# Kernel tuning notes

Hardware: AMD Instinct MI355X
Metric: run time of the kernel (lower is better)

## Reference

```python
import jax, jax.numpy as jnp
import numpy as np

ALIBI_SLOPES = jnp.array([0.6299605249, 0.396850263, 0.25, 0.1574901312,
                          0.0992125657, 0.0625, 0.0393725328, 0.0248031414,
                          0.015625, 0.0098431332, 0.0062007854, 0.00390625],
                         dtype=jnp.float32)
H, D = 12, 64
SCALE = D ** (-0.5)


def setup_inputs() -> dict:
    key = jax.random.key(0)
    ks = jax.random.split(key, 9)
    B, S, E = 4, 2048, 768
    s = 0.02
    return {
        "x": jax.random.normal(ks[0], (B, S, E), dtype=jnp.float32),
        "Wq": jax.random.normal(ks[1], (E, E), dtype=jnp.float32) * s,
        "bq": jnp.zeros((E,), dtype=jnp.float32),
        "Wk": jax.random.normal(ks[2], (E, E), dtype=jnp.float32) * s,
        "bk": jnp.zeros((E,), dtype=jnp.float32),
        "Wv": jax.random.normal(ks[3], (E, E), dtype=jnp.float32) * s,
        "bv": jnp.zeros((E,), dtype=jnp.float32),
        "Wo": jax.random.normal(ks[4], (E, E), dtype=jnp.float32) * s,
        "bo": jnp.zeros((E,), dtype=jnp.float32),
    }


def reference(x, Wq, bq, Wk, bk, Wv, bv, Wo, bo):
    B, S, E = x.shape
    # projections (weights stored input-major: y = x @ W + b)
    q = (x @ Wq + bq).reshape(B, S, H, D).transpose(0, 2, 1, 3)  # [B,H,S,D]
    k = (x @ Wk + bk).reshape(B, S, H, D).transpose(0, 2, 1, 3)
    v = (x @ Wv + bv).reshape(B, S, H, D).transpose(0, 2, 1, 3)

    scores = jnp.einsum('bhqd,bhkd->bhqk', q, k) * SCALE  # [B,H,S,S]

    pos = jnp.arange(S, dtype=jnp.float32)
    a = ALIBI_SLOPES[:, None] * pos[None, :]          # [H,S]
    alibi = a[:, :, None] - a[:, None, :]             # [H,S,S]
    scores = scores + alibi[None]

    causal = jnp.triu(jnp.ones((S, S), dtype=bool), k=1)  # True above diag
    scores = jnp.where(causal[None, None], -jnp.inf, scores)

    attn = jax.nn.softmax(scores, axis=-1)
    o = jnp.einsum('bhqk,bhkd->bhqd', attn, v)  # [B,H,S,D]

    # Faithful to original: view of contiguous (B,H,S,D) buffer as (B,S,E)
    # (head-major flatten, reproducing the original module's reshape).
    o = o.reshape(B, S, E)
    return o @ Wo + bo
```

## Files before the change

### kernel.cpp

```cpp
#include <hip/hip_runtime.h>
#include <hip/hip_bf16.h>
#include <cstdint>
#include <cstddef>

#define B_ 4
#define S_ 2048
#define E_ 768
#define H_ 12
#define D_ 64

typedef __bf16 bf16x8 __attribute__((ext_vector_type(8)));
typedef float f32x4 __attribute__((ext_vector_type(4)));

__constant__ float c_slopes[12] = {
    0.6299605249f, 0.396850263f, 0.25f, 0.1574901312f,
    0.0992125657f, 0.0625f, 0.0393725328f, 0.0248031414f,
    0.015625f, 0.0098431332f, 0.0062007854f, 0.00390625f};

__device__ __forceinline__ unsigned short f2bf_u(float f) {
    unsigned u = __builtin_bit_cast(unsigned, f);
    u += 0x7fffu + ((u >> 16) & 1u);
    return (unsigned short)(u >> 16);
}
__device__ __forceinline__ __bf16 f2bf(float f) {
    unsigned short s = f2bf_u(f);
    return __builtin_bit_cast(__bf16, s);
}

__device__ __forceinline__ void gload_lds16(const void* g, void* l) {
    __builtin_amdgcn_global_load_lds(
        (const __attribute__((address_space(1))) unsigned int*)g,
        (__attribute__((address_space(3))) unsigned int*)l, 16, 0, 0);
}

__global__ __launch_bounds__(256) void prep(
    const float* __restrict__ x, __bf16* __restrict__ xb,
    const float* __restrict__ W0, const float* __restrict__ W1,
    const float* __restrict__ W2, const float* __restrict__ W3,
    __bf16* __restrict__ Wt) {
    __shared__ alignas(16) __bf16 ts[64 * 72];
    const int L = blockIdx.x;
    const int t = threadIdx.x;
    if (L < 6144) {
        int i = (L * 256 + t) * 4;
        float4 v = *(const float4*)(x + i);
        ushort4 o;
        o.x = f2bf_u(v.x); o.y = f2bf_u(v.y); o.z = f2bf_u(v.z); o.w = f2bf_u(v.w);
        *(ushort4*)((unsigned short*)xb + i) = o;
        return;
    }
    const int id = L - 6144;
    const int z = id / 144, rem = id % 144;
    const int k0 = (rem / 12) * 64, n0 = (rem % 12) * 64;
    const float* W = z == 0 ? W0 : z == 1 ? W1 : z == 2 ? W2 : W3;
    __bf16* out = Wt + (size_t)z * E_ * E_;
#pragma unroll
    for (int i = 0; i < 4; i++) {
        int idx = i * 256 + t;
        int row = idx >> 4, c4 = idx & 15;
        float4 v = *(const float4*)(W + (size_t)(k0 + row) * E_ + n0 + c4 * 4);
        ts[(c4 * 4 + 0) * 72 + row] = f2bf(v.x);
        ts[(c4 * 4 + 1) * 72 + row] = f2bf(v.y);
        ts[(c4 * 4 + 2) * 72 + row] = f2bf(v.z);
        ts[(c4 * 4 + 3) * 72 + row] = f2bf(v.w);
    }
    __syncthreads();
#pragma unroll
    for (int i = 0; i < 2; i++) {
        int idx = i * 256 + t;
        int r = idx >> 3, c8 = idx & 7;
        *(uint4*)((unsigned short*)out + (size_t)(n0 + r) * E_ + k0 + c8 * 8) =
            *(const uint4*)((const unsigned short*)ts + r * 72 + c8 * 8);
    }
}

__global__ __launch_bounds__(256, 3) void qkv_gemm(
    const __bf16* __restrict__ A, const __bf16* __restrict__ WtAll,
    const float* __restrict__ b0, const float* __restrict__ b1,
    const float* __restrict__ b2, __bf16* __restrict__ Qb,
    __bf16* __restrict__ Kb, __bf16* __restrict__ Vtb) {
    constexpr int Kd = E_;
    __shared__ alignas(16) __bf16 Asm[2][128 * 32];
    __shared__ alignas(16) __bf16 Bsm[2][3][64 * 32];

    const int t = threadIdx.x;
    const int w = t >> 6, lane = t & 63;
    const int qm = lane & 15, quad = lane >> 4;
    const int m0 = blockIdx.y * 128, n0 = blockIdx.x * 64;
    const int wm = w * 32;

    float bvv[3][4];
    const float* bs[3] = {b0, b1, b2};
#pragma unroll
    for (int z = 0; z < 3; z++)
#pragma unroll
        for (int j = 0; j < 4; j++) bvv[z][j] = bs[z][n0 + j * 16 + qm];

    const int crow = lane >> 2;
    const int ccol = lane & 3;

    f32x4 acc[3][2][4] = {};

    for (int k0 = 0; k0 < Kd; k0 += 64) {
#pragma unroll
        for (int p = 0; p < 2; p++) {
            const int kp = k0 + p * 32;
#pragma unroll
            for (int cc = 0; cc < 2; cc++) {
                int chunk = w * 2 + cc;
                gload_lds16((const unsigned short*)A +
                                (size_t)(m0 + chunk * 16 + crow) * Kd + kp + ccol * 8,
                            Asm[p] + chunk * 512);
            }
#pragma unroll
            for (int e = 0; e < 3; e++) {
                int g = w * 3 + e;
                int z = g >> 2, cz = g & 3;
                gload_lds16((const unsigned short*)WtAll + (size_t)z * Kd * E_ +
                                (size_t)(n0 + cz * 16 + crow) * Kd + kp + ccol * 8,
                            Bsm[p][z] + cz * 512);
            }
        }
        __syncthreads();

#pragma unroll
        for (int p = 0; p < 2; p++) {
            bf16x8 af[2];
#pragma unroll
            for (int i = 0; i < 2; i++)
                af[i] = *(const bf16x8*)(Asm[p] + (wm + i * 16 + qm) * 32 + quad * 8);
#pragma unroll
            for (int z = 0; z < 3; z++) {
                bf16x8 bg[4];
#pragma unroll
                for (int j = 0; j < 4; j++)
                    bg[j] = *(const bf16x8*)(Bsm[p][z] + (j * 16 + qm) * 32 + quad * 8);
#pragma unroll
                for (int i = 0; i < 2; i++)
#pragma unroll
                    for (int j = 0; j < 4; j++)
                        acc[z][i][j] = __builtin_amdgcn_mfma_f32_16x16x32_bf16(
                            af[i], bg[j], acc[z][i][j], 0, 0, 0);
            }
        }
        __syncthreads();
    }

#pragma unroll
    for (int z = 0; z < 3; z++) {
        __bf16* out = z == 0 ? Qb : z == 1 ? Kb : Vtb;
#pragma unroll
        for (int i = 0; i < 2; i++) {
#pragma unroll
            for (int j = 0; j < 4; j++) {
                int col = n0 + j * 16 + qm;
                int rowb = m0 + wm + i * 16 + quad * 4;
                int h = col >> 6, d = col & (D_ - 1);
                if (z == 2) {
                    int b = rowb >> 11, s = rowb & (S_ - 1);
                    unsigned short pk4[4];
#pragma unroll
                    for (int r = 0; r < 4; r++)
                        pk4[r] = f2bf_u(acc[z][i][j][r] + bvv[z][j]);
                    uint2 pv;
                    pv.x = (unsigned)pk4[0] | ((unsigned)pk4[1] << 16);
                    pv.y = (unsigned)pk4[2] | ((unsigned)pk4[3] << 16);
                    *(uint2*)((unsigned short*)out +
                              ((size_t)(b * H_ + h) * D_ + d) * S_ + s) = pv;
                } else {
#pragma unroll
                    for (int r = 0; r < 4; r++) {
                        int row = rowb + r;
                        int b = row >> 11, s = row & (S_ - 1);
                        out[(((size_t)(b * H_ + h)) * S_ + s) * D_ + d] =
                            f2bf(acc[z][i][j][r] + bvv[z][j]);
                    }
                }
            }
        }
    }
}

__global__ __launch_bounds__(256, 3) void gemm_out(
    const __bf16* __restrict__ A, const __bf16* __restrict__ Wt,
    const float* __restrict__ bias, float* __restrict__ outF) {
    constexpr int Kd = E_, N = E_;
    __shared__ alignas(16) __bf16 Asm[2][128 * 32];
    __shared__ alignas(16) __bf16 Bsm[2][64 * 32];

    const int t = threadIdx.x;
    const int w = t >> 6, lane = t & 63;
    const int qm = lane & 15, quad = lane >> 4;
    const int m0 = blockIdx.y * 128, n0 = blockIdx.x * 64;
    const int wm = w * 32;

    float bvv[4];
#pragma unroll
    for (int j = 0; j < 4; j++) bvv[j] = bias[n0 + j * 16 + qm];

    const int crow = lane >> 2;
    const int ccol = lane & 3;

    f32x4 acc[2][4] = {};

    for (int k0 = 0; k0 < Kd; k0 += 64) {
#pragma unroll
        for (int p = 0; p < 2; p++) {
            const int kp = k0 + p * 32;
#pragma unroll
            for (int cc = 0; cc < 2; cc++) {
                int chunk = w * 2 + cc;
                gload_lds16((const unsigned short*)A +
                                (size_t)(m0 + chunk * 16 + crow) * Kd + kp + ccol * 8,
                            Asm[p] + chunk * 512);
            }
            gload_lds16((const unsigned short*)Wt +
                            (size_t)(n0 + w * 16 + crow) * Kd + kp + ccol * 8,
                        Bsm[p] + w * 512);
        }
        __syncthreads();

#pragma unroll
        for (int p = 0; p < 2; p++) {
            bf16x8 af[2], bg[4];
#pragma unroll
            for (int i = 0; i < 2; i++)
                af[i] = *(const bf16x8*)(Asm[p] + (wm + i * 16 + qm) * 32 + quad * 8);
#pragma unroll
            for (int j = 0; j < 4; j++)
                bg[j] = *(const bf16x8*)(Bsm[p] + (j * 16 + qm) * 32 + quad * 8);
#pragma unroll
            for (int i = 0; i < 2; i++)
#pragma unroll
                for (int j = 0; j < 4; j++)
                    acc[i][j] = __builtin_amdgcn_mfma_f32_16x16x32_bf16(
                        af[i], bg[j], acc[i][j], 0, 0, 0);
        }
        __syncthreads();
    }

#pragma unroll
    for (int i = 0; i < 2; i++) {
#pragma unroll
        for (int j = 0; j < 4; j++) {
            int col = n0 + j * 16 + qm;
            int rowb = m0 + wm + i * 16 + quad * 4;
#pragma unroll
            for (int r = 0; r < 4; r++)
                outF[(size_t)(rowb + r) * N + col] = acc[i][j][r] + bvv[j];
        }
    }
}

__global__ __launch_bounds__(256, 6) void attn_k(
    const __bf16* __restrict__ Q, const __bf16* __restrict__ K,
    const __bf16* __restrict__ Vt, __bf16* __restrict__ O) {
    __shared__ alignas(16) __bf16 Ksm[2][64 * 32];
    __shared__ alignas(16) __bf16 Vsm[2][64 * 32];
    __shared__ alignas(16) __bf16 Psm[4 * 16 * 64];

    const int t = threadIdx.x;
    const int w = t >> 6, lane = t & 63;
    const int qm = lane & 15, quad = lane >> 4;
    const int L = blockIdx.x;
    const int r = L & 7;
    const int m = (L >> 3) & 31;
    const int s = L >> 8;
    const int bh = r * 6 + s;
    const int qt = (m + s * 5 + (s >> 1)) & 31;
    const float c2 = c_slopes[bh % H_] * 1.44269504f;
    const size_t base = (size_t)bh * S_ * D_;

    const int bb = qt * 64 + w * 16;
    const __bf16* qp = Q + base + (size_t)(bb + qm) * D_ + quad * 8;
    bf16x8 qf0 = *(const bf16x8*)qp;
    bf16x8 qf1 = *(const bf16x8*)(qp + 32);

    f32x4 oacc[4] = {};
    float lsum = 0.f;
    char* Pb = (char*)Psm + w * 2048;

    const int srow = lane >> 2;
    const int sq = (lane & 3) ^ ((lane >> 3) & 3);
    const unsigned short* Kg = (const unsigned short*)K + base +
                               (size_t)(16 * w + srow) * D_ + sq * 8;
    const unsigned short* Vg = (const unsigned short*)Vt + base +
                               (size_t)(16 * w + srow) * S_ + sq * 8;

    const int cq = (quad ^ ((qm >> 1) & 3)) * 8;
    const int pf = (qm & 7) << 4;

    for (int kt = 0; kt <= qt; kt++) {
#pragma unroll
        for (int h = 0; h < 2; h++) {
            gload_lds16(Kg + (size_t)(kt * 64) * D_ + 32 * h, Ksm[h] + w * 512);
            gload_lds16(Vg + kt * 64 + 32 * h, Vsm[h] + w * 512);
        }
        __syncthreads();

        bf16x8 ak[4][2], bv[4][2];
#pragma unroll
        for (int i = 0; i < 4; i++) {
            ak[i][0] = *(const bf16x8*)(Ksm[0] + (16 * i + qm) * 32 + cq);
            ak[i][1] = *(const bf16x8*)(Ksm[1] + (16 * i + qm) * 32 + cq);
        }
#pragma unroll
        for (int jd = 0; jd < 4; jd++) {
            bv[jd][0] = *(const bf16x8*)(Vsm[0] + (16 * jd + qm) * 32 + cq);
            bv[jd][1] = *(const bf16x8*)(Vsm[1] + (16 * jd + qm) * 32 + cq);
        }

        f32x4 st[4];
#pragma unroll
        for (int i = 0; i < 4; i++) {
            f32x4 zz = {0.f, 0.f, 0.f, 0.f};
            zz = __builtin_amdgcn_mfma_f32_16x16x32_bf16(ak[i][0], qf0, zz, 0, 0, 0);
            zz = __builtin_amdgcn_mfma_f32_16x16x32_bf16(ak[i][1], qf1, zz, 0, 0, 0);
            st[i] = zz;
        }

        const int qi = bb + qm;
        const bool nomask = (kt * 64 + 63) <= bb;
        float ls = 0.f;
        unsigned pk[4][2];
#pragma unroll
        for (int i = 0; i < 4; i++) {
            float bi = -c2 * (float)(kt * 64 + 16 * i + 4 * quad);
            float p[4];
#pragma unroll
            for (int rr = 0; rr < 4; rr++) {
                float tt = st[i][rr] * 0.18033688f + (bi - c2 * (float)rr);
                float pp = __builtin_amdgcn_exp2f(tt);
                if (!nomask) {
                    int key = kt * 64 + 16 * i + 4 * quad + rr;
                    pp = (key > qi) ? 0.f : pp;
                }
                ls += pp;
                p[rr] = pp;
            }
            unsigned u0 = __builtin_bit_cast(unsigned, p[0]) + 0x8000u;
            unsigned u1 = __builtin_bit_cast(unsigned, p[1]) + 0x8000u;
            unsigned u2 = __builtin_bit_cast(unsigned, p[2]) + 0x8000u;
            unsigned u3 = __builtin_bit_cast(unsigned, p[3]) + 0x8000u;
            pk[i][0] = __builtin_amdgcn_perm(u1, u0, 0x07060302u);
            pk[i][1] = __builtin_amdgcn_perm(u3, u2, 0x07060302u);
        }
        lsum += ls;

#pragma unroll
        for (int i = 0; i < 4; i++) {
            uint2 pv; pv.x = pk[i][0]; pv.y = pk[i][1];
            *(uint2*)(Pb + qm * 128 + ((32 * i + 8 * quad) ^ pf)) = pv;
        }

        bf16x8 ap0 = *(const bf16x8*)(Pb + qm * 128 + ((quad * 16) ^ pf));
        bf16x8 ap1 = *(const bf16x8*)(Pb + qm * 128 + ((64 + quad * 16) ^ pf));
#pragma unroll
        for (int jd = 0; jd < 4; jd++) {
            oacc[jd] = __builtin_amdgcn_mfma_f32_16x16x32_bf16(
                ap0, bv[jd][0], oacc[jd], 0, 0, 0);
            oacc[jd] = __builtin_amdgcn_mfma_f32_16x16x32_bf16(
                ap1, bv[jd][1], oacc[jd], 0, 0, 0);
        }

        __syncthreads();
    }

    float lf = lsum;
    lf += __shfl_xor(lf, 16);
    lf += __shfl_xor(lf, 32);
#pragma unroll
    for (int rr = 0; rr < 4; rr++) {
        float lr = __shfl(lf, 4 * quad + rr);
        float inv = 1.0f / lr;
        int qrow = bb + 4 * quad + rr;
#pragma unroll
        for (int jd = 0; jd < 4; jd++)
            O[base + (size_t)qrow * D_ + 16 * jd + qm] =
                f2bf(oacc[jd][rr] * inv);
    }
}

extern "C" void kernel_launch(void* const* d_in, const int* in_sizes, int n_in,
                              void* d_out, int out_size, void* d_ws, size_t ws_size,
                              hipStream_t stream) {
    (void)in_sizes; (void)n_in; (void)out_size; (void)ws_size;
    const float* x  = (const float*)d_in[0];
    const float* Wq = (const float*)d_in[1];
    const float* bq = (const float*)d_in[2];
    const float* Wk = (const float*)d_in[3];
    const float* bk = (const float*)d_in[4];
    const float* Wv = (const float*)d_in[5];
    const float* bv = (const float*)d_in[6];
    const float* Wo = (const float*)d_in[7];
    const float* bo = (const float*)d_in[8];
    float* out = (float*)d_out;

    const size_t n = (size_t)B_ * H_ * S_ * D_;
    __bf16* xb  = (__bf16*)d_ws;
    __bf16* Qb  = xb + n;
    __bf16* Kb  = xb + 2 * n;
    __bf16* Vtb = xb + 3 * n;
    __bf16* Wt  = xb + 4 * n;
    __bf16* Ob  = Qb;

    prep<<<6720, 256, 0, stream>>>(x, xb, Wq, Wk, Wv, Wo, Wt);
    qkv_gemm<<<dim3(12, 64), 256, 0, stream>>>(
        xb, Wt, bq, bk, bv, Qb, Kb, Vtb);
    attn_k<<<1536, 256, 0, stream>>>(Qb, Kb, Vtb, Ob);
    gemm_out<<<dim3(12, 64), 256, 0, stream>>>(
        Ob, Wt + 3 * (size_t)E_ * E_, bo, out);
}
```

Measured before the change: 218.7 us.

## Load V fragments directly from global, peel masked tile, use packed bf16 convert

```diff
diff --git a/kernel.cpp b/kernel.cpp
--- a/kernel.cpp
+++ b/kernel.cpp
@@ -256,7 +256,6 @@
     const __bf16* __restrict__ Q, const __bf16* __restrict__ K,
     const __bf16* __restrict__ Vt, __bf16* __restrict__ O) {
     __shared__ alignas(16) __bf16 Ksm[2][64 * 32];
-    __shared__ alignas(16) __bf16 Vsm[2][64 * 32];
     __shared__ alignas(16) __bf16 Psm[4 * 16 * 64];
 
     const int t = threadIdx.x;
@@ -284,30 +283,38 @@
     const int sq = (lane & 3) ^ ((lane >> 3) & 3);
     const unsigned short* Kg = (const unsigned short*)K + base +
                                (size_t)(16 * w + srow) * D_ + sq * 8;
-    const unsigned short* Vg = (const unsigned short*)Vt + base +
-                               (size_t)(16 * w + srow) * S_ + sq * 8;
+    const __bf16* Vf = Vt + base + (size_t)qm * S_ + quad * 8;
 
     const int cq = (quad ^ ((qm >> 1) & 3)) * 8;
     const int pf = (qm & 7) << 4;
 
-    for (int kt = 0; kt <= qt; kt++) {
-#pragma unroll
-        for (int h = 0; h < 2; h++) {
+    const float scl = 0.18033688f;
+    float cst[4], crr[4];
+#pragma unroll
+    for (int i = 0; i < 4; i++) cst[i] = -c2 * (float)(16 * i + 4 * quad);
+#pragma unroll
+    for (int rr = 0; rr < 4; rr++) crr[rr] = -c2 * (float)rr;
+    const int qi = bb + qm;
+
+    auto body = [&](int kt, bool domask) {
+#pragma unroll
+        for (int h = 0; h < 2; h++)
             gload_lds16(Kg + (size_t)(kt * 64) * D_ + 32 * h, Ksm[h] + w * 512);
-            gload_lds16(Vg + kt * 64 + 32 * h, Vsm[h] + w * 512);
-        }
-        __syncthreads();
-
-        bf16x8 ak[4][2], bv[4][2];
+        __syncthreads();
+
+        bf16x8 bv[4][2];
+#pragma unroll
+        for (int jd = 0; jd < 4; jd++) {
+            const __bf16* vr = Vf + (size_t)(16 * jd) * S_ + kt * 64;
+            bv[jd][0] = *(const bf16x8*)(vr);
+            bv[jd][1] = *(const bf16x8*)(vr + 32);
+        }
+
+        bf16x8 ak[4][2];
 #pragma unroll
         for (int i = 0; i < 4; i++) {
             ak[i][0] = *(const bf16x8*)(Ksm[0] + (16 * i + qm) * 32 + cq);
             ak[i][1] = *(const bf16x8*)(Ksm[1] + (16 * i + qm) * 32 + cq);
-        }
-#pragma unroll
-        for (int jd = 0; jd < 4; jd++) {
-            bv[jd][0] = *(const bf16x8*)(Vsm[0] + (16 * jd + qm) * 32 + cq);
-            bv[jd][1] = *(const bf16x8*)(Vsm[1] + (16 * jd + qm) * 32 + cq);
         }
 
         f32x4 st[4];
@@ -319,31 +326,28 @@
             st[i] = zz;
         }
 
-        const int qi = bb + qm;
-        const bool nomask = (kt * 64 + 63) <= bb;
+        const float kb = -c2 * (float)(kt * 64);
         float ls = 0.f;
         unsigned pk[4][2];
 #pragma unroll
         for (int i = 0; i < 4; i++) {
-            float bi = -c2 * (float)(kt * 64 + 16 * i + 4 * quad);
+            float bi = kb + cst[i];
             float p[4];
 #pragma unroll
             for (int rr = 0; rr < 4; rr++) {
-                float tt = st[i][rr] * 0.18033688f + (bi - c2 * (float)rr);
+                float tt = st[i][rr] * scl + (bi + crr[rr]);
                 float pp = __builtin_amdgcn_exp2f(tt);
-                if (!nomask) {
+                if (domask) {
                     int key = kt * 64 + 16 * i + 4 * quad + rr;
                     pp = (key > qi) ? 0.f : pp;
                 }
                 ls += pp;
                 p[rr] = pp;
             }
-            unsigned u0 = __builtin_bit_cast(unsigned, p[0]) + 0x8000u;
-            unsigned u1 = __builtin_bit_cast(unsigned, p[1]) + 0x8000u;
-            unsigned u2 = __builtin_bit_cast(unsigned, p[2]) + 0x8000u;
-            unsigned u3 = __builtin_bit_cast(unsigned, p[3]) + 0x8000u;
-            pk[i][0] = __builtin_amdgcn_perm(u1, u0, 0x07060302u);
-            pk[i][1] = __builtin_amdgcn_perm(u3, u2, 0x07060302u);
+            asm("v_cvt_pk_bf16_f32 %0, %1, %2"
+                : "=v"(pk[i][0]) : "v"(p[0]), "v"(p[1]));
+            asm("v_cvt_pk_bf16_f32 %0, %1, %2"
+                : "=v"(pk[i][1]) : "v"(p[2]), "v"(p[3]));
         }
         lsum += ls;
 
@@ -364,7 +368,10 @@
         }
 
         __syncthreads();
-    }
+    };
+
+    for (int kt = 0; kt < qt; kt++) body(kt, false);
+    body(qt, true);
 
     float lf = lsum;
     lf += __shfl_xor(lf, 16);
```

Measured after the change: 274.8 us. 25.7% more time.
